# Kernel tuning notes

Hardware: AMD Instinct MI355X
Metric: run time of the kernel (lower is better)

The kernel has to match this reference:

```python
import jax, jax.numpy as jnp
import numpy as np

TOTAL = 409600   # flattened number of (id, rating) pairs across the batch
BATCH = 4096     # number of ragged segments (samples)
VOCAB = 1000000  # sum(field_dims)
DIM = 64         # embed_dim


def setup_inputs() -> dict:
    key = jax.random.key(0)
    k1, k2, k3, k4 = jax.random.split(key, 4)
    ids = jax.random.randint(k1, (TOTAL,), 0, VOCAB, dtype=jnp.int32)
    ratings = jax.random.uniform(k2, (TOTAL,), dtype=jnp.float32)
    segment_ids = jnp.sort(jax.random.randint(k3, (TOTAL,), 0, BATCH, dtype=jnp.int32))
    # Embedding table (xavier_uniform in the original; scale is irrelevant for correctness)
    table = jax.random.normal(k4, (VOCAB, DIM), dtype=jnp.float32) * 0.01
    return {"ids": ids, "ratings": ratings, "segment_ids": segment_ids, "table": table}


def reference(ids, ratings, segment_ids, table):
    # gather rows, scale by ratings, segment-sum over ragged per-sample groups
    emb = table[ids] * ratings[:, None]                      # [TOTAL, DIM]
    out = jax.ops.segment_sum(emb, segment_ids, num_segments=BATCH)  # [BATCH, DIM]
    return out
```

## Files before the change

kernel.cpp:

```cpp
#include <hip/hip_runtime.h>


#define TOTAL 409600
#define BATCH 4096
#define DIM   64

__global__ __launch_bounds__(256) void seg_offsets_kernel(
    const int* __restrict__ seg, int* __restrict__ offsets)
{
    int i = blockIdx.x * blockDim.x + threadIdx.x;
    if (i >= TOTAL) return;
    int cur  = seg[i];
    int prev = (i == 0) ? -1 : seg[i - 1];
    for (int b = prev + 1; b <= cur; ++b) offsets[b] = i;
    if (i == TOTAL - 1) {
        for (int b = cur + 1; b <= BATCH; ++b) offsets[b] = TOTAL;
    }
}

__global__ __launch_bounds__(256) void embed_bag_kernel(
    const int*   __restrict__ ids,
    const float* __restrict__ ratings,
    const int*   __restrict__ offsets,
    const float* __restrict__ table,
    float*       __restrict__ out)
{
    const int wave = threadIdx.x >> 6;
    const int lane = threadIdx.x & 63;
    const int b    = blockIdx.x * 4 + wave;
    const int grp  = lane >> 4;
    const int col  = lane & 15;

    const int start = offsets[b];
    const int end   = offsets[b + 1];
    const int n     = end - start;

    float4 acc = make_float4(0.f, 0.f, 0.f, 0.f);

    constexpr int U = 4;
    const int full = start + (n / (4 * U)) * (4 * U);

    for (int base = start; base < full; base += 4 * U) {
        int   id[U];
        float rt[U];
        #pragma unroll
        for (int u = 0; u < U; ++u) {
            int row = base + 4 * u + grp;
            id[u] = ids[row];
            rt[u] = ratings[row];
        }
        #pragma unroll
        for (int u = 0; u < U; ++u) {
            const float4 v = ((const float4*)(table + (size_t)id[u] * DIM))[col];
            acc.x = fmaf(v.x, rt[u], acc.x);
            acc.y = fmaf(v.y, rt[u], acc.y);
            acc.z = fmaf(v.z, rt[u], acc.z);
            acc.w = fmaf(v.w, rt[u], acc.w);
        }
    }

    for (int base = full; base < end; base += 4) {
        int row = base + grp;
        if (row < end) {
            int   id = ids[row];
            float rt = ratings[row];
            const float4 v = ((const float4*)(table + (size_t)id * DIM))[col];
            acc.x = fmaf(v.x, rt, acc.x);
            acc.y = fmaf(v.y, rt, acc.y);
            acc.z = fmaf(v.z, rt, acc.z);
            acc.w = fmaf(v.w, rt, acc.w);
        }
    }

    #pragma unroll
    for (int m = 16; m <= 32; m <<= 1) {
        acc.x += __shfl_xor(acc.x, m);
        acc.y += __shfl_xor(acc.y, m);
        acc.z += __shfl_xor(acc.z, m);
        acc.w += __shfl_xor(acc.w, m);
    }
    if (grp == 0) {
        ((float4*)(out + (size_t)b * DIM))[col] = acc;
    }
}

extern "C" void kernel_launch(void* const* d_in, const int* in_sizes, int n_in,
                              void* d_out, int out_size, void* d_ws, size_t ws_size,
                              hipStream_t stream) {
    const int*   ids     = (const int*)  d_in[0];
    const float* ratings = (const float*)d_in[1];
    const int*   seg     = (const int*)  d_in[2];
    const float* table   = (const float*)d_in[3];
    float*       out     = (float*)      d_out;
    int*         offsets = (int*)        d_ws;

    seg_offsets_kernel<<<(TOTAL + 255) / 256, 256, 0, stream>>>(seg, offsets);
    embed_bag_kernel<<<BATCH / 4, 256, 0, stream>>>(ids, ratings, offsets, table, out);
}
```

Before: 317.2 us.

## Split each segment across two waves and software-prefetch next index batch

Each segment is now handled by two wavefronts that interleave row groups, with partial sums combined through shared memory, so twice as many waves are in flight for the gather. The main loop also loads the next iteration's ids and ratings before doing the FMAs on the current table rows, to hide index-load latency. Occupancy is raised via a launch_bounds hint. The costs are a block-wide barrier, an LDS reduction, and higher register pressure from the prefetch buffers.

```diff
diff --git a/kernel.cpp b/kernel.cpp
--- a/kernel.cpp
+++ b/kernel.cpp
@@ -18,18 +18,22 @@
     }
 }
 
-__global__ __launch_bounds__(256) void embed_bag_kernel(
+__global__ __launch_bounds__(256, 8) void embed_bag_kernel(
     const int*   __restrict__ ids,
     const float* __restrict__ ratings,
     const int*   __restrict__ offsets,
     const float* __restrict__ table,
     float*       __restrict__ out)
 {
-    const int wave = threadIdx.x >> 6;
-    const int lane = threadIdx.x & 63;
-    const int b    = blockIdx.x * 4 + wave;
-    const int grp  = lane >> 4;
-    const int col  = lane & 15;
+    __shared__ float4 part[2][16];
+
+    const int wid        = threadIdx.x >> 6;
+    const int lane       = threadIdx.x & 63;
+    const int seg_in_blk = wid >> 1;
+    const int half       = wid & 1;
+    const int b          = blockIdx.x * 2 + seg_in_blk;
+    const int grp        = lane >> 4;
+    const int col        = lane & 15;
 
     const int start = offsets[b];
     const int end   = offsets[b + 1];
@@ -38,32 +42,64 @@
     float4 acc = make_float4(0.f, 0.f, 0.f, 0.f);
 
     constexpr int U = 4;
-    const int full = start + (n / (4 * U)) * (4 * U);
 
-    for (int base = start; base < full; base += 4 * U) {
-        int   id[U];
-        float rt[U];
+    const int t     = n - 28 - 4 * half;
+    const int iFull = (t >= 0) ? ((t >> 5) + 1) : 0;
+
+    int   idc[U];
+    float rtc[U];
+    if (iFull > 0) {
         #pragma unroll
         for (int u = 0; u < U; ++u) {
-            int row = base + 4 * u + grp;
-            id[u] = ids[row];
-            rt[u] = ratings[row];
-        }
-        #pragma unroll
-        for (int u = 0; u < U; ++u) {
-            const float4 v = ((const float4*)(table + (size_t)id[u] * DIM))[col];
-            acc.x = fmaf(v.x, rt[u], acc.x);
-            acc.y = fmaf(v.y, rt[u], acc.y);
-            acc.z = fmaf(v.z, rt[u], acc.z);
-            acc.w = fmaf(v.w, rt[u], acc.w);
+            int r = start + 4 * (half + 2 * u) + grp;
+            idc[u] = ids[r];
+            rtc[u] = ratings[r];
         }
     }
 
-    for (int base = full; base < end; base += 4) {
-        int row = base + grp;
-        if (row < end) {
-            int   id = ids[row];
-            float rt = ratings[row];
+    for (int i = 0; i < iFull; ++i) {
+        float4 v0 = ((const float4*)(table + (size_t)idc[0] * DIM))[col];
+        float4 v1 = ((const float4*)(table + (size_t)idc[1] * DIM))[col];
+        float4 v2 = ((const float4*)(table + (size_t)idc[2] * DIM))[col];
+        float4 v3 = ((const float4*)(table + (size_t)idc[3] * DIM))[col];
+
+        int   idn[U] = {0, 0, 0, 0};
+        float rtn[U] = {0.f, 0.f, 0.f, 0.f};
+        if (i + 1 < iFull) {
+            #pragma unroll
+            for (int u = 0; u < U; ++u) {
+                int r = start + 4 * (half + 2 * (U * (i + 1) + u)) + grp;
+                idn[u] = ids[r];
+                rtn[u] = ratings[r];
+            }
+        }
+
+        acc.x = fmaf(v0.x, rtc[0], acc.x);
+        acc.y = fmaf(v0.y, rtc[0], acc.y);
+        acc.z = fmaf(v0.z, rtc[0], acc.z);
+        acc.w = fmaf(v0.w, rtc[0], acc.w);
+        acc.x = fmaf(v1.x, rtc[1], acc.x);
+        acc.y = fmaf(v1.y, rtc[1], acc.y);
+        acc.z = fmaf(v1.z, rtc[1], acc.z);
+        acc.w = fmaf(v1.w, rtc[1], acc.w);
+        acc.x = fmaf(v2.x, rtc[2], acc.x);
+        acc.y = fmaf(v2.y, rtc[2], acc.y);
+        acc.z = fmaf(v2.z, rtc[2], acc.z);
+        acc.w = fmaf(v2.w, rtc[2], acc.w);
+        acc.x = fmaf(v3.x, rtc[3], acc.x);
+        acc.y = fmaf(v3.y, rtc[3], acc.y);
+        acc.z = fmaf(v3.z, rtc[3], acc.z);
+        acc.w = fmaf(v3.w, rtc[3], acc.w);
+
+        #pragma unroll
+        for (int u = 0; u < U; ++u) { idc[u] = idn[u]; rtc[u] = rtn[u]; }
+    }
+
+    for (int q = half + 2 * (U * iFull); 4 * q < n; q += 2) {
+        int r = start + 4 * q + grp;
+        if (r < end) {
+            int   id = ids[r];
+            float rt = ratings[r];
             const float4 v = ((const float4*)(table + (size_t)id * DIM))[col];
             acc.x = fmaf(v.x, rt, acc.x);
             acc.y = fmaf(v.y, rt, acc.y);
@@ -79,7 +115,12 @@
         acc.z += __shfl_xor(acc.z, m);
         acc.w += __shfl_xor(acc.w, m);
     }
-    if (grp == 0) {
+
+    if (half == 1 && grp == 0) part[seg_in_blk][col] = acc;
+    __syncthreads();
+    if (half == 0 && grp == 0) {
+        float4 o = part[seg_in_blk][col];
+        acc.x += o.x; acc.y += o.y; acc.z += o.z; acc.w += o.w;
         ((float4*)(out + (size_t)b * DIM))[col] = acc;
     }
 }
@@ -95,5 +136,5 @@
     int*         offsets = (int*)        d_ws;
 
     seg_offsets_kernel<<<(TOTAL + 255) / 256, 256, 0, stream>>>(seg, offsets);
-    embed_bag_kernel<<<BATCH / 4, 256, 0, stream>>>(ids, ratings, offsets, table, out);
+    embed_bag_kernel<<<BATCH / 2, 256, 0, stream>>>(ids, ratings, offsets, table, out);
 }
```

Result: no change. 317.8 us (+0.2%).
